# Optimization experiments

Measured on AMD Instinct MI355X. Metric: run time of the kernel, lower is better.

## Reference

```python
import jax, jax.numpy as jnp
import numpy as np

N, F = 12288, 512
NEG_INF = jnp.float32(-1e9)  # matches Keras BaseDenseAttention mask additive constant


def setup_inputs() -> dict:
    key = jax.random.key(0)
    k1, k2 = jax.random.split(key)
    features = jax.random.normal(k1, (N, F), dtype=jnp.float32)
    A = jax.random.randint(k2, (N, N), 0, 2).astype(jnp.int32)
    return {"features": features, "A": A}


def reference(features, A):
    # Keras Attention with query=key=value=dropout(features); dropout is identity
    # at inference. use_scale=False -> plain dot-product scores, no 1/sqrt(d).
    scores = jnp.einsum("nf,mf->nm", features, features)          # [N, N]
    scores = jnp.where(A > 0, scores, NEG_INF)                    # mask non-edges
    attn = jax.nn.softmax(scores, axis=-1)                        # softmax over keys
    return jnp.einsum("nm,mf->nf", attn, features)                # [N, F]
```

## Files before the change

### kernel.cpp

```cpp
#include <hip/hip_runtime.h>
#include <cstddef>
#include <cstdint>

#define NN 12288
#define FF 512
#define NKT (NN / 128)

using half8 = __attribute__((ext_vector_type(8))) _Float16;
using half4 = __attribute__((ext_vector_type(4))) _Float16;
using f32x4 = __attribute__((ext_vector_type(4))) float;

constexpr float MASK_NEG = -1e9f;

__device__ __forceinline__ void gll16(const void* g, void* l) {
    __builtin_amdgcn_global_load_lds((const __attribute__((address_space(1))) void*)g,
                                     (__attribute__((address_space(3))) void*)l, 16, 0, 0);
}

__global__ __launch_bounds__(256)
void prep_feat_kernel(const float* __restrict__ in, _Float16* __restrict__ feath,
                      _Float16* __restrict__ featT) {
    __shared__ float tile[32][33];
    const int bi = blockIdx.x;
    const int bj = blockIdx.y;
    const int r  = threadIdx.x >> 3;
    const int c4 = (threadIdx.x & 7) << 2;
    float4 v = *reinterpret_cast<const float4*>(in + (size_t)(bi * 32 + r) * FF + bj * 32 + c4);
    tile[r][c4 + 0] = v.x; tile[r][c4 + 1] = v.y; tile[r][c4 + 2] = v.z; tile[r][c4 + 3] = v.w;
    half4 hr;
    hr[0] = (_Float16)v.x; hr[1] = (_Float16)v.y; hr[2] = (_Float16)v.z; hr[3] = (_Float16)v.w;
    *reinterpret_cast<half4*>(feath + (size_t)(bi * 32 + r) * FF + bj * 32 + c4) = hr;
    __syncthreads();
    half4 h;
#pragma unroll
    for (int k = 0; k < 4; ++k) h[k] = (_Float16)tile[c4 + k][r];
    *reinterpret_cast<half4*>(featT + (size_t)(bj * 32 + r) * NN + bi * 32 + c4) = h;
}

__global__ void cvt_feat_kernel(const float* __restrict__ in, _Float16* __restrict__ out) {
    const size_t i = ((size_t)blockIdx.x * blockDim.x + threadIdx.x) * 8;
    float4 x = *reinterpret_cast<const float4*>(in + i);
    float4 y = *reinterpret_cast<const float4*>(in + i + 4);
    half8 h;
    h[0] = (_Float16)x.x; h[1] = (_Float16)x.y; h[2] = (_Float16)x.z; h[3] = (_Float16)x.w;
    h[4] = (_Float16)y.x; h[5] = (_Float16)y.y; h[6] = (_Float16)y.z; h[7] = (_Float16)y.w;
    *reinterpret_cast<half8*>(out + i) = h;
}

__global__ __launch_bounds__(256)
void gemm1_exp(const _Float16* __restrict__ feath, const int* __restrict__ Amat,
               _Float16* __restrict__ Pmat, float* __restrict__ m_t, _Float16* __restrict__ s_t) {
    __shared__ alignas(16) _Float16 As[2][128 * 32];
    __shared__ alignas(16) _Float16 Bs[2][128 * 32];
    __shared__ alignas(16) float rowmax2[128][2];
    __shared__ alignas(16) float rowsum2[128][2];

    const int tid = threadIdx.x, lane = tid & 63, wid = tid >> 6;
    const int g = lane >> 4, a = lane & 15;
    const int wr = wid >> 1, wc = wid & 1;
    const int row0 = blockIdx.x * 128, col0 = blockIdx.y * 128;

    f32x4 acc[4][4];
#pragma unroll
    for (int i = 0; i < 4; ++i)
#pragma unroll
        for (int j = 0; j < 4; ++j) acc[i][j] = f32x4{0.f, 0.f, 0.f, 0.f};

    const int lr = lane >> 2;
    const int li = (lane & 3) * 8;

    auto stage = [&](int buf, int t) {
#pragma unroll
        for (int c = 0; c < 2; ++c) {
            const int ch = wid * 2 + c;
            gll16(feath + (size_t)(row0 + ch * 16 + lr) * FF + t * 32 + li, &As[buf][ch * 512]);
            gll16(feath + (size_t)(col0 + ch * 16 + lr) * FF + t * 32 + li, &Bs[buf][ch * 512]);
        }
    };

    const int  arow_base = row0 + 64 * wr + 4 * g;
    const int  acol      = col0 + 64 * wc + a;
    unsigned long long bits = 0ULL;
    int p0, p1, p2, p3;
    {
        const size_t rb = (size_t)arow_base * NN + acol;
        p0 = Amat[rb]; p1 = Amat[rb + 16]; p2 = Amat[rb + 32]; p3 = Amat[rb + 48];
    }

    stage(0, 0);
    __syncthreads();
    int buf = 0;
#pragma unroll
    for (int t = 0; t < 16; ++t) {
        if (t + 1 < 16) stage(buf ^ 1, t + 1);
        bits |= (unsigned long long)(p0 > 0) << (4 * t + 0);
        bits |= (unsigned long long)(p1 > 0) << (4 * t + 1);
        bits |= (unsigned long long)(p2 > 0) << (4 * t + 2);
        bits |= (unsigned long long)(p3 > 0) << (4 * t + 3);
        if (t + 1 < 16) {
            const int rfn = (t + 1) >> 2, rrn = (t + 1) & 3;
            const size_t rb = (size_t)(arow_base + 16 * rfn + rrn) * NN + acol;
            p0 = Amat[rb]; p1 = Amat[rb + 16]; p2 = Amat[rb + 32]; p3 = Amat[rb + 48];
        }
        half8 af[4], bf[4];
#pragma unroll
        for (int rf = 0; rf < 4; ++rf)
            af[rf] = *reinterpret_cast<const half8*>(&As[buf][(64 * wr + 16 * rf + a) * 32 + 8 * g]);
#pragma unroll
        for (int cf = 0; cf < 4; ++cf)
            bf[cf] = *reinterpret_cast<const half8*>(&Bs[buf][(64 * wc + 16 * cf + a) * 32 + 8 * g]);
#pragma unroll
        for (int rf = 0; rf < 4; ++rf)
#pragma unroll
            for (int cf = 0; cf < 4; ++cf)
                acc[rf][cf] = __builtin_amdgcn_mfma_f32_16x16x32_f16(af[rf], bf[cf], acc[rf][cf], 0, 0, 0);
        __syncthreads();
        buf ^= 1;
    }

#pragma unroll
    for (int rf = 0; rf < 4; ++rf)
#pragma unroll
        for (int r = 0; r < 4; ++r)
#pragma unroll
            for (int cf = 0; cf < 4; ++cf) {
                const unsigned long long bit = (bits >> (rf * 16 + r * 4 + cf)) & 1ULL;
                acc[rf][cf][r] = bit ? acc[rf][cf][r] : MASK_NEG;
            }

#pragma unroll
    for (int rf = 0; rf < 4; ++rf)
#pragma unroll
        for (int r = 0; r < 4; ++r) {
            float v = fmaxf(fmaxf(acc[rf][0][r], acc[rf][1][r]), fmaxf(acc[rf][2][r], acc[rf][3][r]));
            v = fmaxf(v, __shfl_xor(v, 1, 16));
            v = fmaxf(v, __shfl_xor(v, 2, 16));
            v = fmaxf(v, __shfl_xor(v, 4, 16));
            v = fmaxf(v, __shfl_xor(v, 8, 16));
            if (a == 0) rowmax2[64 * wr + 16 * rf + 4 * g + r][wc] = v;
        }
    __syncthreads();

#pragma unroll
    for (int rf = 0; rf < 4; ++rf)
#pragma unroll
        for (int r = 0; r < 4; ++r) {
            const int lrow = 64 * wr + 16 * rf + 4 * g + r;
            const float mt = fmaxf(rowmax2[lrow][0], rowmax2[lrow][1]);
            const size_t rbase = (size_t)(row0 + lrow) * NN + col0 + 64 * wc + a;
            float ps = 0.f;
#pragma unroll
            for (int cf = 0; cf < 4; ++cf) {
                const float p = __expf(acc[rf][cf][r] - mt);
                ps += p;
                Pmat[rbase + 16 * cf] = (_Float16)p;
            }
            ps += __shfl_xor(ps, 1, 16);
            ps += __shfl_xor(ps, 2, 16);
            ps += __shfl_xor(ps, 4, 16);
            ps += __shfl_xor(ps, 8, 16);
            if (a == 0) rowsum2[lrow][wc] = ps;
        }
    __syncthreads();
    if (tid < 128) {
        m_t[(size_t)blockIdx.y * NN + row0 + tid] = fmaxf(rowmax2[tid][0], rowmax2[tid][1]);
        s_t[(size_t)blockIdx.y * NN + row0 + tid] = (_Float16)(rowsum2[tid][0] + rowsum2[tid][1]);
    }
}

__global__ __launch_bounds__(256)
void stats_kernel(const float* __restrict__ m_t, const _Float16* __restrict__ s_t,
                  _Float16* __restrict__ sc_t, float* __restrict__ l_row) {
    const int r = blockIdx.x * 256 + threadIdx.x;
    float m = -3.0e38f;
#pragma unroll 4
    for (int kt = 0; kt < NKT; ++kt) m = fmaxf(m, m_t[(size_t)kt * NN + r]);
    float l = 0.f;
#pragma unroll 4
    for (int kt = 0; kt < NKT; ++kt) {
        const float e = __expf(m_t[(size_t)kt * NN + r] - m);
        sc_t[(size_t)kt * NN + r] = (_Float16)e;
        l += e * (float)s_t[(size_t)kt * NN + r];
    }
    l_row[r] = l;
}

__global__ __launch_bounds__(256)
void gemm2_scale(const _Float16* __restrict__ Pmat, const _Float16* __restrict__ featT,
                 const _Float16* __restrict__ sc_t, const float* __restrict__ l_row,
                 float* __restrict__ out) {
    __shared__ alignas(16) _Float16 As[2][128 * 32];
    __shared__ alignas(16) _Float16 Bs[2][64 * 32];

    const int tid = threadIdx.x, lane = tid & 63, wid = tid >> 6;
    const int g = lane >> 4, a = lane & 15;
    const int wr = wid >> 1, wc = wid & 1;
    const int row0 = blockIdx.x * 128, col0 = blockIdx.y * 64;

    f32x4 acc[4][2];
#pragma unroll
    for (int i = 0; i < 4; ++i) { acc[i][0] = f32x4{0.f,0.f,0.f,0.f}; acc[i][1] = f32x4{0.f,0.f,0.f,0.f}; }

    const int lr = lane >> 2;
    const int li = (lane & 3) * 8;
    const size_t scbase = row0 + 64 * wr + a;

    auto stage = [&](int buf, int t) {
#pragma unroll
        for (int c = 0; c < 2; ++c) {
            const int ch = wid * 2 + c;
            gll16(Pmat + (size_t)(row0 + ch * 16 + lr) * NN + t * 32 + li, &As[buf][ch * 512]);
        }
        gll16(featT + (size_t)(col0 + wid * 16 + lr) * NN + t * 32 + li, &Bs[buf][wid * 512]);
    };

    _Float16 pend[4], sc[4];
#pragma unroll
    for (int rf = 0; rf < 4; ++rf) pend[rf] = sc_t[scbase + 16 * rf];

    stage(0, 0);
    __syncthreads();
    int buf = 0;
    for (int t = 0; t < 384; ++t) {
        if ((t & 3) == 0) {
#pragma unroll
            for (int rf = 0; rf < 4; ++rf) sc[rf] = pend[rf];
            const int ktn = (t >> 2) + 1;
            if (ktn < NKT) {
#pragma unroll
                for (int rf = 0; rf < 4; ++rf)
                    pend[rf] = sc_t[(size_t)ktn * NN + scbase + 16 * rf];
            }
        }
        if (t + 1 < 384) stage(buf ^ 1, t + 1);
        half8 af[4], bf[2];
#pragma unroll
        for (int rf = 0; rf < 4; ++rf) {
            af[rf] = *reinterpret_cast<const half8*>(&As[buf][(64 * wr + 16 * rf + a) * 32 + 8 * g]);
            af[rf] = af[rf] * sc[rf];
        }
#pragma unroll
        for (int cf = 0; cf < 2; ++cf)
            bf[cf] = *reinterpret_cast<const half8*>(&Bs[buf][(32 * wc + 16 * cf + a) * 32 + 8 * g]);
#pragma unroll
        for (int rf = 0; rf < 4; ++rf)
#pragma unroll
            for (int cf = 0; cf < 2; ++cf)
                acc[rf][cf] = __builtin_amdgcn_mfma_f32_16x16x32_f16(af[rf], bf[cf], acc[rf][cf], 0, 0, 0);
        __syncthreads();
        buf ^= 1;
    }

#pragma unroll
    for (int rf = 0; rf < 4; ++rf)
#pragma unroll
        for (int r = 0; r < 4; ++r) {
            const int grow = row0 + 64 * wr + 16 * rf + 4 * g + r;
            const float il = 1.0f / l_row[grow];
#pragma unroll
            for (int cf = 0; cf < 2; ++cf) {
                const int gcol = col0 + 32 * wc + 16 * cf + a;
                out[(size_t)grow * FF + gcol] = acc[rf][cf][r] * il;
            }
        }
}

constexpr int BM_ = 64;
constexpr int BN_ = 64;
constexpr int KV_STRIDE = 520;

template<bool RH>
__global__ __launch_bounds__(512, 2)
void attn_flash(const float* __restrict__ featf, const _Float16* __restrict__ feath,
                const int* __restrict__ Amat, float* __restrict__ out) {
    __shared__ alignas(16) _Float16 kv[BN_ * KV_STRIDE];
    __shared__ alignas(16) _Float16 pbuf[BM_][72];
    __shared__ alignas(16) float pmax[BM_][2];
    __shared__ alignas(16) float psum[BM_][2];
    __shared__ alignas(16) float m_s[BM_];
    __shared__ alignas(16) float l_s[BM_];
    __shared__ alignas(16) float rscale[BM_];

    const int tid  = threadIdx.x;
    const int lane = tid & 63;
    const int wid  = tid >> 6;
    const int g    = lane >> 4;
    const int a    = lane & 15;
    const int rg   = wid >> 1;
    const int ch   = wid & 1;
    const int qrow0 = blockIdx.x * BM_;

    half8 qf[16];
    {
        const int qr = qrow0 + 16 * rg + a;
#pragma unroll
        for (int ks = 0; ks < 16; ++ks) {
            const int f0 = 32 * ks + 8 * g;
            if constexpr (RH) {
                qf[ks] = *reinterpret_cast<const half8*>(feath + (size_t)qr * FF + f0);
            } else {
                const float* sp = featf + (size_t)qr * FF + f0;
                float4 x = *reinterpret_cast<const float4*>(sp);
                float4 y = *reinterpret_cast<const float4*>(sp + 4);
                half8 h;
                h[0] = (_Float16)x.x; h[1] = (_Float16)x.y; h[2] = (_Float16)x.z; h[3] = (_Float16)x.w;
                h[4] = (_Float16)y.x; h[5] = (_Float16)y.y; h[6] = (_Float16)y.z; h[7] = (_Float16)y.w;
                qf[ks] = h;
            }
        }
    }

    f32x4 acc[4][4];
#pragma unroll
    for (int i = 0; i < 4; ++i)
#pragma unroll
        for (int j = 0; j < 4; ++j) acc[i][j] = f32x4{0.f, 0.f, 0.f, 0.f};

    if (tid < BM_) { m_s[tid] = -INFINITY; l_s[tid] = 0.f; }
    __syncthreads();

    for (int kt = 0; kt < NN / BN_; ++kt) {
        const int key0 = kt * BN_;
#pragma unroll
        for (int i = 0; i < 8; ++i) {
            const int flat8 = tid + i * 512;
            const int key   = flat8 >> 6;
            const int b     = flat8 & 63;
            const int slot  = (b + (key >> 3)) & 63;
            _Float16* dst = &kv[key * KV_STRIDE + slot * 8];
            if constexpr (RH) {
                *reinterpret_cast<half8*>(dst) =
                    *reinterpret_cast<const half8*>(feath + (size_t)(key0 + key) * FF + b * 8);
            } else {
                const float* sp = featf + (size_t)(key0 + key) * FF + b * 8;
                float4 x = *reinterpret_cast<const float4*>(sp);
                float4 y = *reinterpret_cast<const float4*>(sp + 4);
                half8 h;
                h[0] = (_Float16)x.x; h[1] = (_Float16)x.y; h[2] = (_Float16)x.z; h[3] = (_Float16)x.w;
                h[4] = (_Float16)y.x; h[5] = (_Float16)y.y; h[6] = (_Float16)y.z; h[7] = (_Float16)y.w;
                *reinterpret_cast<half8*>(dst) = h;
            }
        }

        int am[2][4];
#pragma unroll
        for (int fc = 0; fc < 2; ++fc)
#pragma unroll
            for (int r = 0; r < 4; ++r) {
                const int arow = qrow0 + 16 * rg + 4 * g + r;
                const int acol = key0 + 32 * ch + 16 * fc + a;
                am[fc][r] = Amat[(size_t)arow * NN + acol];
            }
        __syncthreads();

        f32x4 s0{0.f, 0.f, 0.f, 0.f}, s1{0.f, 0.f, 0.f, 0.f};
        const int bk0 = 32 * ch + a;
        const int bk1 = bk0 + 16;
        const int kb0 = bk0 >> 3;
        const int kb1 = bk1 >> 3;
        const _Float16* kr0 = &kv[bk0 * KV_STRIDE];
        const _Float16* kr1 = &kv[bk1 * KV_STRIDE];
#pragma unroll
        for (int ks = 0; ks < 16; ++ks) {
            const int b = 4 * ks + g;
            const half8 bf0 = *reinterpret_cast<const half8*>(kr0 + (((b + kb0) & 63) << 3));
            const half8 bf1 = *reinterpret_cast<const half8*>(kr1 + (((b + kb1) & 63) << 3));
            s0 = __builtin_amdgcn_mfma_f32_16x16x32_f16(qf[ks], bf0, s0, 0, 0, 0);
            s1 = __builtin_amdgcn_mfma_f32_16x16x32_f16(qf[ks], bf1, s1, 0, 0, 0);
        }

        float sv[2][4];
#pragma unroll
        for (int r = 0; r < 4; ++r) {
            sv[0][r] = (am[0][r] > 0) ? s0[r] : MASK_NEG;
            sv[1][r] = (am[1][r] > 0) ? s1[r] : MASK_NEG;
        }
#pragma unroll
        for (int r = 0; r < 4; ++r) {
            float v = fmaxf(sv[0][r], sv[1][r]);
            v = fmaxf(v, __shfl_xor(v, 1, 16));
            v = fmaxf(v, __shfl_xor(v, 2, 16));
            v = fmaxf(v, __shfl_xor(v, 4, 16));
            v = fmaxf(v, __shfl_xor(v, 8, 16));
            if (a == 0) pmax[16 * rg + 4 * g + r][ch] = v;
        }
        __syncthreads();

#pragma unroll
        for (int r = 0; r < 4; ++r) {
            const int row = 16 * rg + 4 * g + r;
            const float mo = m_s[row];
            const float mn = fmaxf(mo, fmaxf(pmax[row][0], pmax[row][1]));
            const float p0 = __expf(sv[0][r] - mn);
            const float p1 = __expf(sv[1][r] - mn);
            pbuf[row][32 * ch + a]      = (_Float16)p0;
            pbuf[row][32 * ch + 16 + a] = (_Float16)p1;
            float ssum = p0 + p1;
            ssum += __shfl_xor(ssum, 1, 16);
            ssum += __shfl_xor(ssum, 2, 16);
            ssum += __shfl_xor(ssum, 4, 16);
            ssum += __shfl_xor(ssum, 8, 16);
            if (a == 0) psum[row][ch] = ssum;
        }
        __syncthreads();

        if (tid < BM_) {
            const float mo = m_s[tid];
            const float mn = fmaxf(mo, fmaxf(pmax[tid][0], pmax[tid][1]));
            const float sc = __expf(mo - mn);
            l_s[tid] = l_s[tid] * sc + psum[tid][0] + psum[tid][1];
            m_s[tid] = mn;
            rscale[tid] = sc;
        }
        __syncthreads();

#pragma unroll
        for (int rf = 0; rf < 4; ++rf) {
            const float4 scv = *reinterpret_cast<const float4*>(&rscale[16 * rf + 4 * g]);
#pragma unroll
            for (int cf = 0; cf < 4; ++cf) {
                acc[rf][cf][0] *= scv.x; acc[rf][cf][1] *= scv.y;
                acc[rf][cf][2] *= scv.z; acc[rf][cf][3] *= scv.w;
            }
        }
#pragma unroll
        for (int kk = 0; kk < 2; ++kk) {
            half8 af[4];
#pragma unroll
            for (int rf = 0; rf < 4; ++rf)
                af[rf] = *reinterpret_cast<const half8*>(&pbuf[16 * rf + a][32 * kk + 8 * g]);
            const int keybase = 32 * kk + 8 * g;
#pragma unroll
            for (int cf = 0; cf < 4; ++cf) {
                const int col  = 64 * wid + 16 * cf + a;
                const int slot = (((col >> 3) + 4 * kk + g) & 63);
                const _Float16* vb = &kv[(size_t)keybase * KV_STRIDE + (slot << 3) + (col & 7)];
                half8 bf;
#pragma unroll
                for (int j = 0; j < 8; ++j)
                    bf[j] = vb[j * KV_STRIDE];
#pragma unroll
                for (int rf = 0; rf < 4; ++rf)
                    acc[rf][cf] = __builtin_amdgcn_mfma_f32_16x16x32_f16(af[rf], bf, acc[rf][cf], 0, 0, 0);
            }
        }
        __syncthreads();
    }

#pragma unroll
    for (int rf = 0; rf < 4; ++rf) {
        const float4 lv = *reinterpret_cast<const float4*>(&l_s[16 * rf + 4 * g]);
        const float inv[4] = {1.f / lv.x, 1.f / lv.y, 1.f / lv.z, 1.f / lv.w};
#pragma unroll
        for (int cf = 0; cf < 4; ++cf) {
            const int col = 64 * wid + 16 * cf + a;
#pragma unroll
            for (int r = 0; r < 4; ++r) {
                out[(size_t)(qrow0 + 16 * rf + 4 * g + r) * FF + col] = acc[rf][cf][r] * inv[r];
            }
        }
    }
}

extern "C" void kernel_launch(void* const* d_in, const int* in_sizes, int n_in,
                              void* d_out, int out_size, void* d_ws, size_t ws_size,
                              hipStream_t stream) {
    const float* features = (const float*)d_in[0];
    const int*   Amat     = (const int*)d_in[1];
    float*       out      = (float*)d_out;

    const size_t P_bytes   = (size_t)NN * NN * 2;
    const size_t f16_bytes = (size_t)NN * FF * 2;
    const size_t sct_bytes = (size_t)NKT * NN * 2;
    const size_t st_bytes  = (size_t)NKT * NN * 2;
    const size_t l_bytes   = (size_t)NN * 4;
    const size_t total     = P_bytes + 2 * f16_bytes + sct_bytes + st_bytes + l_bytes;

    if (ws_size >= total) {
        char* w = (char*)d_ws;
        _Float16* Pmat  = (_Float16*)w;   w += P_bytes;
        _Float16* feath = (_Float16*)w;   w += f16_bytes;
        _Float16* featT = (_Float16*)w;   w += f16_bytes;
        _Float16* sc_t  = (_Float16*)w;   w += sct_bytes;
        _Float16* s_t   = (_Float16*)w;   w += st_bytes;
        float*    l_row = (float*)w;

        float* m_t = (float*)d_out;

        prep_feat_kernel<<<dim3(NN / 32, FF / 32), 256, 0, stream>>>(features, feath, featT);
        gemm1_exp<<<dim3(NN / 128, NN / 128), 256, 0, stream>>>(feath, Amat, Pmat, m_t, s_t);
        stats_kernel<<<NN / 256, 256, 0, stream>>>(m_t, s_t, sc_t, l_row);
        gemm2_scale<<<dim3(NN / 128, FF / 64), 256, 0, stream>>>(Pmat, featT, sc_t, l_row, out);
    } else if (ws_size >= f16_bytes) {
        _Float16* feath = (_Float16*)d_ws;
        cvt_feat_kernel<<<(NN * FF) / (256 * 8), 256, 0, stream>>>(features, feath);
        attn_flash<true><<<NN / BM_, 512, 0, stream>>>(features, feath, Amat, out);
    } else {
        attn_flash<false><<<NN / BM_, 512, 0, stream>>>(features, nullptr, Amat, out);
    }
}
```

Baseline: 875.1 us.

## Triple-buffer gemm1 LDS pipeline and stage P tile through LDS for coalesced stores

Moves the score GEMM's LDS staging from double to triple buffering. Manual vmcnt waits plus one barrier per k-step replace the trailing __syncthreads, so two tiles stay in flight. Adjacency loads are deferred by two iterations to keep them off the critical path. The exp'd P tile is written to padded LDS and then stored to global as 16-byte vectors instead of scattered 2-byte stores. This uses more LDS, which may cut occupancy, and the hand-set vmcnt counts must match the issued loads exactly.

After: 837.5 us. 1.04x faster.

```diff
diff --git a/kernel.cpp b/kernel.cpp
--- a/kernel.cpp
+++ b/kernel.cpp
@@ -16,6 +16,13 @@
     __builtin_amdgcn_global_load_lds((const __attribute__((address_space(1))) void*)g,
                                      (__attribute__((address_space(3))) void*)l, 16, 0, 0);
 }
+
+#define PHASE(N)                                                        \
+    do {                                                                \
+        asm volatile("s_waitcnt vmcnt(" #N ")" ::: "memory");           \
+        __builtin_amdgcn_s_barrier();                                   \
+        __builtin_amdgcn_sched_barrier(0);                              \
+    } while (0)
 
 __global__ __launch_bounds__(256)
 void prep_feat_kernel(const float* __restrict__ in, _Float16* __restrict__ feath,
@@ -50,10 +57,12 @@
 __global__ __launch_bounds__(256)
 void gemm1_exp(const _Float16* __restrict__ feath, const int* __restrict__ Amat,
                _Float16* __restrict__ Pmat, float* __restrict__ m_t, _Float16* __restrict__ s_t) {
-    __shared__ alignas(16) _Float16 As[2][128 * 32];
-    __shared__ alignas(16) _Float16 Bs[2][128 * 32];
+    __shared__ alignas(16) _Float16 smem[3 * 4096 * 2];
     __shared__ alignas(16) float rowmax2[128][2];
     __shared__ alignas(16) float rowsum2[128][2];
+
+    _Float16* As = smem;
+    _Float16* Bs = smem + 12288;
 
     const int tid = threadIdx.x, lane = tid & 63, wid = tid >> 6;
     const int g = lane >> 4, a = lane & 15;
@@ -73,50 +82,54 @@
 #pragma unroll
         for (int c = 0; c < 2; ++c) {
             const int ch = wid * 2 + c;
-            gll16(feath + (size_t)(row0 + ch * 16 + lr) * FF + t * 32 + li, &As[buf][ch * 512]);
-            gll16(feath + (size_t)(col0 + ch * 16 + lr) * FF + t * 32 + li, &Bs[buf][ch * 512]);
+            gll16(feath + (size_t)(row0 + ch * 16 + lr) * FF + t * 32 + li, &As[buf * 4096 + ch * 512]);
+            gll16(feath + (size_t)(col0 + ch * 16 + lr) * FF + t * 32 + li, &Bs[buf * 4096 + ch * 512]);
         }
     };
 
     const int  arow_base = row0 + 64 * wr + 4 * g;
     const int  acol      = col0 + 64 * wc + a;
     unsigned long long bits = 0ULL;
-    int p0, p1, p2, p3;
-    {
-        const size_t rb = (size_t)arow_base * NN + acol;
-        p0 = Amat[rb]; p1 = Amat[rb + 16]; p2 = Amat[rb + 32]; p3 = Amat[rb + 48];
-    }
+    int p[2][4];
 
     stage(0, 0);
-    __syncthreads();
-    int buf = 0;
+    stage(1, 1);
 #pragma unroll
     for (int t = 0; t < 16; ++t) {
-        if (t + 1 < 16) stage(buf ^ 1, t + 1);
-        bits |= (unsigned long long)(p0 > 0) << (4 * t + 0);
-        bits |= (unsigned long long)(p1 > 0) << (4 * t + 1);
-        bits |= (unsigned long long)(p2 > 0) << (4 * t + 2);
-        bits |= (unsigned long long)(p3 > 0) << (4 * t + 3);
-        if (t + 1 < 16) {
-            const int rfn = (t + 1) >> 2, rrn = (t + 1) & 3;
-            const size_t rb = (size_t)(arow_base + 16 * rfn + rrn) * NN + acol;
-            p0 = Amat[rb]; p1 = Amat[rb + 16]; p2 = Amat[rb + 32]; p3 = Amat[rb + 48];
-        }
+        if (t == 0)      PHASE(4);
+        else if (t < 15) PHASE(8);
+        else             PHASE(4);
+        if (t >= 2) {
+            const int tc = t - 2;
+#pragma unroll
+            for (int cf = 0; cf < 4; ++cf)
+                bits |= (unsigned long long)(p[tc & 1][cf] > 0) << (4 * tc + cf);
+        }
+        const int cb = t % 3;
         half8 af[4], bf[4];
 #pragma unroll
         for (int rf = 0; rf < 4; ++rf)
-            af[rf] = *reinterpret_cast<const half8*>(&As[buf][(64 * wr + 16 * rf + a) * 32 + 8 * g]);
+            af[rf] = *reinterpret_cast<const half8*>(&As[cb * 4096 + (64 * wr + 16 * rf + a) * 32 + 8 * g]);
 #pragma unroll
         for (int cf = 0; cf < 4; ++cf)
-            bf[cf] = *reinterpret_cast<const half8*>(&Bs[buf][(64 * wc + 16 * cf + a) * 32 + 8 * g]);
+            bf[cf] = *reinterpret_cast<const half8*>(&Bs[cb * 4096 + (64 * wc + 16 * cf + a) * 32 + 8 * g]);
 #pragma unroll
         for (int rf = 0; rf < 4; ++rf)
 #pragma unroll
             for (int cf = 0; cf < 4; ++cf)
                 acc[rf][cf] = __builtin_amdgcn_mfma_f32_16x16x32_f16(af[rf], bf[cf], acc[rf][cf], 0, 0, 0);
-        __syncthreads();
-        buf ^= 1;
-    }
+        {
+            const size_t rb = (size_t)(arow_base + 16 * (t >> 2) + (t & 3)) * NN + acol;
+#pragma unroll
+            for (int cf = 0; cf < 4; ++cf) p[t & 1][cf] = Amat[rb + 16 * cf];
+        }
+        if (t + 2 < 16) stage((t + 2) % 3, t + 2);
+    }
+#pragma unroll
+    for (int tc = 14; tc < 16; ++tc)
+#pragma unroll
+        for (int cf = 0; cf < 4; ++cf)
+            bits |= (unsigned long long)(p[tc & 1][cf] > 0) << (4 * tc + cf);
 
 #pragma unroll
     for (int rf = 0; rf < 4; ++rf)
@@ -141,19 +154,19 @@
         }
     __syncthreads();
 
+    _Float16* ptile = smem;
 #pragma unroll
     for (int rf = 0; rf < 4; ++rf)
 #pragma unroll
         for (int r = 0; r < 4; ++r) {
             const int lrow = 64 * wr + 16 * rf + 4 * g + r;
             const float mt = fmaxf(rowmax2[lrow][0], rowmax2[lrow][1]);
-            const size_t rbase = (size_t)(row0 + lrow) * NN + col0 + 64 * wc + a;
             float ps = 0.f;
 #pragma unroll
             for (int cf = 0; cf < 4; ++cf) {
-                const float p = __expf(acc[rf][cf][r] - mt);
-                ps += p;
-                Pmat[rbase + 16 * cf] = (_Float16)p;
+                const float pv = __expf(acc[rf][cf][r] - mt);
+                ps += pv;
+                ptile[lrow * 136 + 64 * wc + 16 * cf + a] = (_Float16)pv;
             }
             ps += __shfl_xor(ps, 1, 16);
             ps += __shfl_xor(ps, 2, 16);
@@ -162,6 +175,15 @@
             if (a == 0) rowsum2[lrow][wc] = ps;
         }
     __syncthreads();
+
+#pragma unroll
+    for (int j = 0; j < 8; ++j) {
+        const int flat = tid + 256 * j;
+        const int r  = flat >> 4;
+        const int c  = (flat & 15) * 8;
+        *reinterpret_cast<half8*>(Pmat + (size_t)(row0 + r) * NN + col0 + c) =
+            *reinterpret_cast<const half8*>(&ptile[r * 136 + c]);
+    }
     if (tid < 128) {
         m_t[(size_t)blockIdx.y * NN + row0 + tid] = fmaxf(rowmax2[tid][0], rowmax2[tid][1]);
         s_t[(size_t)blockIdx.y * NN + row0 + tid] = (_Float16)(rowsum2[tid][0] + rowsum2[tid][1]);
```
